# Performance work log

Measured on AMD Instinct MI355X. Metric: run time of the kernel, lower is better.

The kernel has to match this reference:

```python
import jax, jax.numpy as jnp
import numpy as np

N_R, N_V, D, E_RR, L, G = 50000, 2000, 128, 800000, 3, 32


def setup_inputs() -> dict:
    key = jax.random.key(0)
    ks = jax.random.split(key, 10)
    x_real = jax.random.normal(ks[0], (N_R, D), dtype=jnp.float32)
    x_virtual = jax.random.normal(ks[1], (N_V, D), dtype=jnp.float32)
    # params: [num_layers, 3 relations (r_to_r, r_to_v, v_to_r), D, D]
    W_root = jax.random.normal(ks[2], (L, 3, D, D), dtype=jnp.float32) * 0.05
    W_nbr = jax.random.normal(ks[3], (L, 3, D, D), dtype=jnp.float32) * 0.05
    bias = jax.random.normal(ks[4], (L, 3, D), dtype=jnp.float32) * 0.05
    edge_rr = jax.random.randint(ks[5], (2, E_RR), 0, N_R)
    # one virtual-node edge per real node (hierarchical virtual nodes)
    src_rv = jnp.arange(N_R)
    dst_rv = jax.random.randint(ks[6], (N_R,), 0, N_V)
    edge_rv = jnp.stack([src_rv, dst_rv])          # real -> virtual
    edge_vr = jnp.stack([dst_rv, src_rv])          # virtual -> real
    batch_real = jnp.sort(jax.random.randint(ks[7], (N_R,), 0, G))
    return {
        "x_real": x_real, "x_virtual": x_virtual,
        "W_root": W_root, "W_nbr": W_nbr, "bias": bias,
        "edge_rr": edge_rr, "edge_rv": edge_rv, "edge_vr": edge_vr,
        "batch_real": batch_real,
    }


def _graph_conv(x_src, x_dst, src, dst, Wr, Wn, b, n_dst):
    # PyG GraphConv-style: root transform + sum-aggregated neighbor messages
    msg = jax.ops.segment_sum(x_src[src] @ Wn, dst, num_segments=n_dst)
    return x_dst @ Wr + msg + b


def _forward(x_real, x_virtual, W_root, W_nbr, bias, edge_rr, edge_rv, edge_vr, batch_real):
    x_r, x_v = x_real, x_virtual
    n_r, n_v = x_r.shape[0], x_v.shape[0]
    for l in range(W_root.shape[0]):
        # HeteroConv with aggr='sum': sum relation outputs per destination type
        c_rr = _graph_conv(x_r, x_r, edge_rr[0], edge_rr[1], W_root[l, 0], W_nbr[l, 0], bias[l, 0], n_r)
        c_vr = _graph_conv(x_v, x_r, edge_vr[0], edge_vr[1], W_root[l, 2], W_nbr[l, 2], bias[l, 2], n_r)
        c_rv = _graph_conv(x_r, x_v, edge_rv[0], edge_rv[1], W_root[l, 1], W_nbr[l, 1], bias[l, 1], n_v)
        # activation + dropout (eval mode -> identity)
        x_r = jax.nn.relu(c_rr + c_vr)
        x_v = jax.nn.relu(c_rv)
    # mean readout over real nodes per graph
    counts = jax.ops.segment_sum(jnp.ones((n_r,), x_r.dtype), batch_real, num_segments=G)
    graph_emb = jax.ops.segment_sum(x_r, batch_real, num_segments=G) / jnp.maximum(counts, 1.0)[:, None]
    return x_r, graph_emb


def reference(x_real, x_virtual, W_root, W_nbr, bias, edge_rr, edge_rv, edge_vr, batch_real):
    node_embedding, graph_embedding = _forward(
        x_real, x_virtual, W_root, W_nbr, bias, edge_rr, edge_rv, edge_vr, batch_real)
    return node_embedding, graph_embedding
```

## Files before the change

### kernel.cpp

```cpp
#include <hip/hip_runtime.h>
#include <hip/hip_bf16.h>

#define N_R   50000
#define N_V   2000
#define DIM   128
#define E_RR  800000
#define NLAY  3
#define NGR   32
#define RCHUNK 16

#define BUKD  128
#define NBUK  391
#define CHKE  2048
#define NCHK  391

typedef __attribute__((ext_vector_type(8))) short bf16x8;
typedef __attribute__((ext_vector_type(4))) float f32x4;
typedef __attribute__((ext_vector_type(2))) float f32x2;
typedef __attribute__((ext_vector_type(8))) unsigned char u8x8;

__device__ __forceinline__ ushort f2bf(float f) {
    unsigned u = __builtin_bit_cast(unsigned, f);
    unsigned r = (u + 0x7fffu + ((u >> 16) & 1u)) >> 16;
    return (ushort)r;
}
__device__ __forceinline__ float bf2f(ushort h) {
    unsigned u = ((unsigned)h) << 16;
    return __builtin_bit_cast(float, u);
}
__device__ __forceinline__ int lbound(const int* __restrict__ a, int n, int key) {
    int lo = 0, hi = n;
    while (lo < hi) { int mid = (lo + hi) >> 1; if (a[mid] < key) lo = mid + 1; else hi = mid; }
    return lo;
}

__device__ __forceinline__ void acc_u8row(
    unsigned w0, unsigned w1, float s,
    f32x2& a01, f32x2& a23, f32x2& a45, f32x2& a67)
{
    f32x2 sc = {s, s};
    a01 += sc * (f32x2){(float)(w0 & 0xffu), (float)((w0 >> 8) & 0xffu)};
    a23 += sc * (f32x2){(float)((w0 >> 16) & 0xffu), (float)(w0 >> 24)};
    a45 += sc * (f32x2){(float)(w1 & 0xffu), (float)((w1 >> 8) & 0xffu)};
    a67 += sc * (f32x2){(float)((w1 >> 16) & 0xffu), (float)(w1 >> 24)};
}

__global__ __launch_bounds__(256) void hist_kernel(
    const int* __restrict__ dst, int n, int* __restrict__ cnt)
{
    int i = blockIdx.x * 256 + threadIdx.x;
    if (i < n) atomicAdd(&cnt[dst[i]], 1);
}

__global__ __launch_bounds__(256) void scan_single_kernel(
    const int* __restrict__ cnt, int n, int nedges,
    int* __restrict__ rowptr, int* __restrict__ cursor)
{
    __shared__ int lds[256];
    __shared__ int carry;
    int t = threadIdx.x;
    if (t == 0) carry = 0;
    __syncthreads();
    for (int base = 0; base < n; base += 256) {
        int i = base + t;
        int v = (i < n) ? cnt[i] : 0;
        lds[t] = v;
        __syncthreads();
        #pragma unroll
        for (int off = 1; off < 256; off <<= 1) {
            int u = (t >= off) ? lds[t - off] : 0;
            __syncthreads();
            lds[t] += u;
            __syncthreads();
        }
        int excl = carry + lds[t] - v;
        if (i < n) {
            rowptr[i] = excl;
            if (cursor) cursor[i] = excl;
        }
        __syncthreads();
        if (t == 255) carry += lds[255];
        __syncthreads();
    }
    if (t == 0) rowptr[n] = nedges;
}

__global__ __launch_bounds__(256) void fill_kernel(
    const int* __restrict__ src, const int* __restrict__ dst, int n,
    int* __restrict__ cursor, int* __restrict__ col)
{
    int i = blockIdx.x * 256 + threadIdx.x;
    if (i < n) {
        int p = atomicAdd(&cursor[dst[i]], 1);
        col[p] = src[i];
    }
}

__global__ __launch_bounds__(256) void bkt_count_kernel(
    const int* __restrict__ dst, unsigned short* __restrict__ cnt2d)
{
    __shared__ int h[NBUK];
    int t = threadIdx.x, c = blockIdx.x;
    for (int i = t; i < NBUK; i += 256) h[i] = 0;
    __syncthreads();
    int e0 = c * CHKE, e1 = min(e0 + CHKE, E_RR);
    for (int e = e0 + t; e < e1; e += 256) atomicAdd(&h[dst[e] >> 7], 1);
    __syncthreads();
    for (int i = t; i < NBUK; i += 256)
        cnt2d[(size_t)c * NBUK + i] = (unsigned short)h[i];
}

__global__ __launch_bounds__(64) void bkt_prefix_kernel(
    const unsigned short* __restrict__ cnt2d,
    unsigned short* __restrict__ rel2d, int* __restrict__ tot)
{
    int b = blockIdx.x, lane = threadIdx.x;
    int base = 0;
    for (int c0 = 0; c0 < NCHK; c0 += 64) {
        int c = c0 + lane;
        int v = (c < NCHK) ? (int)cnt2d[(size_t)c * NBUK + b] : 0;
        int s = v;
        #pragma unroll
        for (int off = 1; off < 64; off <<= 1) {
            int u = __shfl_up(s, off);
            if (lane >= off) s += u;
        }
        if (c < NCHK) rel2d[(size_t)c * NBUK + b] = (unsigned short)(base + s - v);
        base += __shfl(s, 63);
    }
    if (lane == 0) tot[b] = base;
}

__global__ __launch_bounds__(256) void bkt_scatter_kernel(
    const int* __restrict__ src, const int* __restrict__ dst,
    const unsigned short* __restrict__ rel2d, const int* __restrict__ bstart,
    unsigned* __restrict__ ebuf)
{
    __shared__ int cur[NBUK];
    int t = threadIdx.x, c = blockIdx.x;
    for (int i = t; i < NBUK; i += 256)
        cur[i] = bstart[i] + (int)rel2d[(size_t)c * NBUK + i];
    __syncthreads();
    int e0 = c * CHKE, e1 = min(e0 + CHKE, E_RR);
    for (int e = e0 + t; e < e1; e += 256) {
        int d = dst[e];
        int p = atomicAdd(&cur[d >> 7], 1);
        ebuf[p] = ((unsigned)d << 16) | (unsigned)src[e];
    }
}

__global__ __launch_bounds__(256) void bkt_fine_kernel(
    const unsigned* __restrict__ ebuf, const int* __restrict__ bstart,
    int* __restrict__ rowptr, int* __restrict__ col)
{
    __shared__ int cnt[BUKD];
    __shared__ int sc[BUKD];
    __shared__ int cur[BUKD];
    int b = blockIdx.x, t = threadIdx.x;
    int s0 = bstart[b], s1 = bstart[b + 1];
    if (t < BUKD) cnt[t] = 0;
    __syncthreads();
    for (int e = s0 + t; e < s1; e += 256)
        atomicAdd(&cnt[(ebuf[e] >> 16) & (BUKD - 1)], 1);
    __syncthreads();
    if (t < BUKD) sc[t] = cnt[t];
    __syncthreads();
    #pragma unroll
    for (int off = 1; off < BUKD; off <<= 1) {
        int v = (t < BUKD && t >= off) ? sc[t - off] : 0;
        __syncthreads();
        if (t < BUKD) sc[t] += v;
        __syncthreads();
    }
    if (t < BUKD) {
        int ex = sc[t] - cnt[t];
        int d = b * BUKD + t;
        if (d < N_R) rowptr[d] = s0 + ex;
        cur[t] = ex;
    }
    if (b == NBUK - 1 && t == 0) rowptr[N_R] = E_RR;
    __syncthreads();
    for (int e = s0 + t; e < s1; e += 256) {
        unsigned pk = ebuf[e];
        int p = atomicAdd(&cur[(pk >> 16) & (BUKD - 1)], 1);
        col[s0 + p] = (int)(pk & 0xffffu);
    }
}

__global__ __launch_bounds__(256) void quant_input_kernel(
    const float* __restrict__ in, unsigned char* __restrict__ q,
    float2* __restrict__ meta)
{
    int w = (blockIdx.x * 256 + threadIdx.x) >> 6;
    int lane = threadIdx.x & 63;
    if (w >= N_R) return;
    float2 v = *(const float2*)(in + (size_t)w * DIM + lane * 2);
    float mn = fminf(v.x, v.y), mx = fmaxf(v.x, v.y);
    #pragma unroll
    for (int off = 1; off < 64; off <<= 1) {
        mn = fminf(mn, __shfl_xor(mn, off));
        mx = fmaxf(mx, __shfl_xor(mx, off));
    }
    float range = mx - mn;
    float inv = (range > 0.f) ? 255.f / range : 0.f;
    unsigned q0 = (unsigned)__float2int_rn((v.x - mn) * inv);
    unsigned q1 = (unsigned)__float2int_rn((v.y - mn) * inv);
    *(ushort*)(q + (size_t)w * DIM + lane * 2) = (ushort)(q0 | (q1 << 8));
    if (lane == 0) meta[w] = make_float2(range / 255.f, mn);
}

__global__ __launch_bounds__(256) void build_wt_kernel(
    const float* __restrict__ Wroot, const float* __restrict__ Wnbr,
    ushort* __restrict__ WT)
{
    int idx = blockIdx.x * 256 + threadIdx.x;
    if (idx >= NLAY * DIM * 2 * DIM) return;
    int k = idx & 255;
    int n = (idx >> 8) & 127;
    int l = idx >> 15;
    float v;
    if (k < DIM) {
        const float* base = Wroot + (size_t)l * 3 * DIM * DIM;
        v = base[(size_t)k * DIM + n] + base[(size_t)(2 * DIM + k) * DIM + n];
    } else {
        v = Wnbr[((size_t)l * 3 * DIM + (k - DIM)) * DIM + n];
    }
    WT[idx] = f2bf(v);
}

__global__ __launch_bounds__(256) void combine_b_kernel(
    const float* __restrict__ bias, float* __restrict__ bc)
{
    int idx = blockIdx.x * 256 + threadIdx.x;
    if (idx >= NLAY * DIM) return;
    int l = idx / DIM;
    int rest = idx - l * DIM;
    const float* base = bias + (size_t)l * 3 * DIM;
    bc[idx] = base[rest] + base[2 * DIM + rest];
}

__global__ __launch_bounds__(256) void vlayer_kernel(
    const int* __restrict__ rowptr, const int* __restrict__ col,
    const unsigned char* __restrict__ Xq, const float2* __restrict__ Xm,
    const float* __restrict__ xv,
    const float* __restrict__ Wn2, const float* __restrict__ Wr1,
    const float* __restrict__ Wn1, const float* __restrict__ b1,
    float* __restrict__ Tv, float* __restrict__ xv_next, int doNext)
{
    __shared__ float part[4 * DIM];
    __shared__ float arv_s[DIM];
    int v = blockIdx.x;
    int t = threadIdx.x;
    int wave = t >> 6, lane = t & 63;

    if (doNext) {
        int beg = rowptr[v], end = rowptr[v + 1];
        float a0 = 0.f, a1 = 0.f, msum = 0.f;
        for (int e = beg + wave; e < end; e += 4) {
            int c = col[e];
            float2 m = Xm[c];
            uchar2 u = *(const uchar2*)(Xq + (size_t)c * DIM + lane * 2);
            a0 += m.x * (float)u.x;
            a1 += m.x * (float)u.y;
            msum += m.y;
        }
        part[wave * DIM + lane * 2 + 0] = a0 + msum;
        part[wave * DIM + lane * 2 + 1] = a1 + msum;
        __syncthreads();
        if (t < DIM)
            arv_s[t] = part[t] + part[DIM + t] + part[2 * DIM + t] + part[3 * DIM + t];
        __syncthreads();
    }

    const float* arow = xv + (size_t)v * DIM;
    if (t < DIM) {
        float tacc = 0.f;
        #pragma unroll 8
        for (int k = 0; k < DIM; ++k)
            tacc += arow[k] * Wn2[(size_t)k * DIM + t];
        Tv[(size_t)v * DIM + t] = tacc;
    } else if (doNext) {
        int c = t - DIM;
        float nacc = 0.f;
        #pragma unroll 4
        for (int k = 0; k < DIM; ++k)
            nacc += arow[k] * Wr1[(size_t)k * DIM + c]
                  + arv_s[k] * Wn1[(size_t)k * DIM + c];
        xv_next[(size_t)v * DIM + c] = fmaxf(nacc + b1[c], 0.f);
    }
}

__global__ __launch_bounds__(256) void fused_layer_kernel(
    const int* __restrict__ rowptr, const int* __restrict__ col,
    const unsigned char* __restrict__ Xq, const float2* __restrict__ Xm,
    const ushort* __restrict__ WT,
    const float* __restrict__ Tv,  const int* __restrict__ vmap,
    const float* __restrict__ bias,
    float* __restrict__ outF,
    unsigned char* __restrict__ Xq_out, float2* __restrict__ Xm_out, int M)
{
    __shared__ ushort a2[16 * DIM];
    __shared__ float ost[16 * DIM];
    int t = threadIdx.x;

    int wave = t >> 6, lane = t & 63;
    int rlo = lane & 15, hi = lane >> 4;
    int row0 = blockIdx.x * 16;
    int arowc = min(row0 + rlo, M - 1);
    float2 am = Xm[arowc];
    bf16x8 afr[8];
    #pragma unroll
    for (int j = 0; j < 4; ++j) {
        u8x8 uv = *(const u8x8*)(Xq + (size_t)arowc * DIM + 32 * j + 8 * hi);
        bf16x8 f;
        #pragma unroll
        for (int q = 0; q < 8; ++q)
            f[q] = (short)f2bf(am.x * (float)uv[q] + am.y);
        afr[j] = f;
    }
    int vr[4];
    #pragma unroll
    for (int i = 0; i < 4; ++i)
        vr[i] = vmap[min(row0 + 4 * hi + i, M - 1)];

    {
        int g = t >> 3;
        int li = t & 7;
        int row = g >> 1;
        int half = g & 1;
        int drow = min(row0 + row, M - 1);
        int beg = rowptr[drow], end = rowptr[drow + 1];
        const unsigned char* XH = Xq + half * 64 + li * 8;
        f32x2 a01 = {0.f, 0.f}, a23 = {0.f, 0.f};
        f32x2 a45 = {0.f, 0.f}, a67 = {0.f, 0.f};
        float msum = 0.f;
        int e = beg;
        for (; e + 3 < end; e += 4) {
            int c0 = col[e + 0], c1 = col[e + 1], c2 = col[e + 2], c3 = col[e + 3];
            float2 m0 = Xm[c0], m1 = Xm[c1], m2 = Xm[c2], m3 = Xm[c3];
            uint2 d0 = *(const uint2*)(XH + (size_t)c0 * DIM);
            uint2 d1 = *(const uint2*)(XH + (size_t)c1 * DIM);
            uint2 d2 = *(const uint2*)(XH + (size_t)c2 * DIM);
            uint2 d3 = *(const uint2*)(XH + (size_t)c3 * DIM);
            acc_u8row(d0.x, d0.y, m0.x, a01, a23, a45, a67);
            acc_u8row(d1.x, d1.y, m1.x, a01, a23, a45, a67);
            acc_u8row(d2.x, d2.y, m2.x, a01, a23, a45, a67);
            acc_u8row(d3.x, d3.y, m3.x, a01, a23, a45, a67);
            msum += (m0.y + m1.y) + (m2.y + m3.y);
        }
        for (; e < end; ++e) {
            int c0 = col[e];
            float2 m0 = Xm[c0];
            uint2 d0 = *(const uint2*)(XH + (size_t)c0 * DIM);
            acc_u8row(d0.x, d0.y, m0.x, a01, a23, a45, a67);
            msum += m0.y;
        }
        bf16x8 pk;
        pk[0] = (short)f2bf(a01.x + msum);
        pk[1] = (short)f2bf(a01.y + msum);
        pk[2] = (short)f2bf(a23.x + msum);
        pk[3] = (short)f2bf(a23.y + msum);
        pk[4] = (short)f2bf(a45.x + msum);
        pk[5] = (short)f2bf(a45.y + msum);
        pk[6] = (short)f2bf(a67.x + msum);
        pk[7] = (short)f2bf(a67.y + msum);
        int byte = row * 256 + ((half * 128 + li * 16) ^ ((row & 7) << 4));
        *(bf16x8*)((char*)a2 + byte) = pk;
    }
    __syncthreads();

    #pragma unroll
    for (int jj = 0; jj < 4; ++jj) {
        int byte = rlo * 256 + ((64 * jj + 16 * hi) ^ ((rlo & 7) << 4));
        afr[4 + jj] = *(const bf16x8*)((const char*)a2 + byte);
    }

    f32x4 acc[2];
    #pragma unroll
    for (int n = 0; n < 2; ++n) acc[n] = (f32x4){0.f, 0.f, 0.f, 0.f};

    #pragma unroll
    for (int n = 0; n < 2; ++n) {
        int nt = wave * 2 + n;
        const ushort* wrow = WT + (size_t)(nt * 16 + rlo) * (2 * DIM);
        #pragma unroll
        for (int j = 0; j < 8; ++j) {
            bf16x8 bfr = *(const bf16x8*)(wrow + 32 * j + 8 * hi);
            acc[n] = __builtin_amdgcn_mfma_f32_16x16x32_bf16(afr[j], bfr, acc[n], 0, 0, 0);
        }
    }

    if (outF) {
        #pragma unroll
        for (int n = 0; n < 2; ++n) {
            int ncol = (wave * 2 + n) * 16 + rlo;
            float bv = bias[ncol];
            #pragma unroll
            for (int i = 0; i < 4; ++i) {
                int orow = row0 + 4 * hi + i;
                if (orow >= M) continue;
                float v = acc[n][i] + bv + Tv[(size_t)vr[i] * DIM + ncol];
                outF[(size_t)orow * DIM + ncol] = fmaxf(v, 0.f);
            }
        }
    } else {
        #pragma unroll
        for (int n = 0; n < 2; ++n) {
            int ncol = (wave * 2 + n) * 16 + rlo;
            float bv = bias[ncol];
            #pragma unroll
            for (int i = 0; i < 4; ++i) {
                float v = acc[n][i] + bv + Tv[(size_t)vr[i] * DIM + ncol];
                ost[(4 * hi + i) * DIM + ncol] = fmaxf(v, 0.f);
            }
        }
        __syncthreads();
        int g16 = t >> 4;
        int li16 = t & 15;
        int orow = row0 + g16;
        float4 f0 = *(const float4*)(ost + g16 * DIM + li16 * 8);
        float4 f1 = *(const float4*)(ost + g16 * DIM + li16 * 8 + 4);
        float mn = fminf(fminf(fminf(f0.x, f0.y), fminf(f0.z, f0.w)),
                         fminf(fminf(f1.x, f1.y), fminf(f1.z, f1.w)));
        float mx = fmaxf(fmaxf(fmaxf(f0.x, f0.y), fmaxf(f0.z, f0.w)),
                         fmaxf(fmaxf(f1.x, f1.y), fmaxf(f1.z, f1.w)));
        #pragma unroll
        for (int off = 1; off < 16; off <<= 1) {
            mn = fminf(mn, __shfl_xor(mn, off, 16));
            mx = fmaxf(mx, __shfl_xor(mx, off, 16));
        }
        float range = mx - mn;
        float inv = (range > 0.f) ? 255.f / range : 0.f;
        if (orow < M) {
            u8x8 qv;
            qv[0] = (unsigned char)__float2int_rn((f0.x - mn) * inv);
            qv[1] = (unsigned char)__float2int_rn((f0.y - mn) * inv);
            qv[2] = (unsigned char)__float2int_rn((f0.z - mn) * inv);
            qv[3] = (unsigned char)__float2int_rn((f0.w - mn) * inv);
            qv[4] = (unsigned char)__float2int_rn((f1.x - mn) * inv);
            qv[5] = (unsigned char)__float2int_rn((f1.y - mn) * inv);
            qv[6] = (unsigned char)__float2int_rn((f1.z - mn) * inv);
            qv[7] = (unsigned char)__float2int_rn((f1.w - mn) * inv);
            *(u8x8*)(Xq_out + (size_t)orow * DIM + li16 * 8) = qv;
            if (li16 == 0) Xm_out[orow] = make_float2(range / 255.f, mn);
        }
    }
}

__global__ __launch_bounds__(256) void readout_kernel(
    const float* __restrict__ xr, const int* __restrict__ batch,
    float* __restrict__ gsum, int nrows)
{
    __shared__ float lds[256 * 4];
    int g = blockIdx.x / RCHUNK;
    int chunk = blockIdx.x % RCHUNK;
    int lo = lbound(batch, nrows, g);
    int hi = lbound(batch, nrows, g + 1);
    int len = hi - lo;
    if (len == 0) return;
    int per = (len + RCHUNK - 1) / RCHUNK;
    int r0 = lo + chunk * per;
    int r1 = min(r0 + per, hi);

    int t = threadIdx.x;
    int c4 = (t & 31) << 2;
    int rsub = t >> 5;

    float4 acc = make_float4(0.f, 0.f, 0.f, 0.f);
    for (int r = r0 + rsub; r < r1; r += 8) {
        float4 v = *(const float4*)(xr + (size_t)r * DIM + c4);
        acc.x += v.x; acc.y += v.y; acc.z += v.z; acc.w += v.w;
    }
    *(float4*)(lds + t * 4) = acc;
    __syncthreads();
    if (rsub == 0) {
        float4 s = make_float4(0.f, 0.f, 0.f, 0.f);
        #pragma unroll
        for (int j = 0; j < 8; ++j) {
            float4 v = *(const float4*)(lds + (j * 32 + t) * 4);
            s.x += v.x; s.y += v.y; s.z += v.z; s.w += v.w;
        }
        atomicAdd(&gsum[(size_t)g * DIM + c4 + 0], s.x);
        atomicAdd(&gsum[(size_t)g * DIM + c4 + 1], s.y);
        atomicAdd(&gsum[(size_t)g * DIM + c4 + 2], s.z);
        atomicAdd(&gsum[(size_t)g * DIM + c4 + 3], s.w);
    }
}

__global__ __launch_bounds__(256) void finalize_kernel(
    const float* __restrict__ gsum, const int* __restrict__ batch,
    float* __restrict__ out, int nrows)
{
    int idx = blockIdx.x * 256 + threadIdx.x;
    if (idx >= NGR * DIM) return;
    int g = idx >> 7;
    int lo = lbound(batch, nrows, g);
    int hi = lbound(batch, nrows, g + 1);
    float c = fmaxf((float)(hi - lo), 1.f);
    out[idx] = gsum[idx] / c;
}

extern "C" void kernel_launch(void* const* d_in, const int* in_sizes, int n_in,
                              void* d_out, int out_size, void* d_ws, size_t ws_size,
                              hipStream_t stream)
{
    const float* x_real    = (const float*)d_in[0];
    const float* x_virtual = (const float*)d_in[1];
    const float* W_root    = (const float*)d_in[2];
    const float* W_nbr     = (const float*)d_in[3];
    const float* bias      = (const float*)d_in[4];
    const int*   edge_rr   = (const int*)d_in[5];
    const int*   edge_rv   = (const int*)d_in[6];
    const int*   edge_vr   = (const int*)d_in[7];
    const int*   batch     = (const int*)d_in[8];

    float* out = (float*)d_out;

    float2* meta0 = (float2*)d_ws;
    float2* meta1 = meta0 + N_R;
    float2* meta2 = meta1 + N_R;
    float*  Tv    = (float*)(meta2 + N_R);
    float*  xv_a  = Tv   + (size_t)N_V * DIM;
    float*  xv_b  = xv_a + (size_t)N_V * DIM;
    float*  bc    = xv_b + (size_t)N_V * DIM;
    float*  gsum  = bc   + (size_t)NLAY * DIM;
    ushort* WT    = (ushort*)(gsum + NGR * DIM);
    int* iws       = (int*)(WT + (size_t)NLAY * DIM * 2 * DIM);
    int* rowptr_rr = iws;
    int* col_rr    = rowptr_rr + N_R + 1;
    int* cnt_v     = col_rr + E_RR;
    int* rowptr_rv = cnt_v + N_V;
    int* cursor_rv = rowptr_rv + N_V + 1;
    int* col_rv    = cursor_rv + N_V;
    int* tot       = col_rv + N_R;
    int* bstart    = tot + NBUK;
    unsigned short* cnt2d = (unsigned short*)(bstart + NBUK + 1);
    unsigned short* rel2d = cnt2d + (size_t)NCHK * NBUK;
    unsigned* ebuf = (unsigned*)(rel2d + (size_t)NCHK * NBUK + 2);
    unsigned char* Q0 = (unsigned char*)(ebuf + E_RR);
    unsigned char* Q1 = Q0 + (size_t)N_R * DIM;
    unsigned char* Q2 = Q1 + (size_t)N_R * DIM;

    const int* rr_src = edge_rr;
    const int* rr_dst = edge_rr + E_RR;
    const int* rv_src = edge_rv;
    const int* rv_dst = edge_rv + N_R;

    bkt_count_kernel<<<NCHK, 256, 0, stream>>>(rr_dst, cnt2d);
    bkt_prefix_kernel<<<NBUK, 64, 0, stream>>>(cnt2d, rel2d, tot);
    scan_single_kernel<<<1, 256, 0, stream>>>(tot, NBUK, E_RR, bstart, nullptr);
    bkt_scatter_kernel<<<NCHK, 256, 0, stream>>>(rr_src, rr_dst, rel2d, bstart, ebuf);
    bkt_fine_kernel<<<NBUK, 256, 0, stream>>>(ebuf, bstart, rowptr_rr, col_rr);

    hipMemsetAsync(cnt_v, 0, (size_t)N_V * sizeof(int), stream);
    hist_kernel<<<(N_R + 255) / 256, 256, 0, stream>>>(rv_dst, N_R, cnt_v);
    scan_single_kernel<<<1, 256, 0, stream>>>(cnt_v, N_V, N_R, rowptr_rv, cursor_rv);
    fill_kernel<<<(N_R + 255) / 256, 256, 0, stream>>>(rv_src, rv_dst, N_R, cursor_rv, col_rv);

    build_wt_kernel<<<(NLAY * DIM * 2 * DIM + 255) / 256, 256, 0, stream>>>(W_root, W_nbr, WT);
    combine_b_kernel<<<(NLAY * DIM + 255) / 256, 256, 0, stream>>>(bias, bc);
    quant_input_kernel<<<(N_R * 64 + 255) / 256, 256, 0, stream>>>(x_real, Q0, meta0);

    unsigned char* Qcur = Q0;  float2* Mcur = meta0;
    const float* cur_xv = x_virtual;

    for (int l = 0; l < NLAY; ++l) {
        const float* Wn1 = W_nbr + ((size_t)l * 3 + 1) * DIM * DIM;
        const float* Wn2 = W_nbr + ((size_t)l * 3 + 2) * DIM * DIM;
        const float* Wr1 = W_root + ((size_t)l * 3 + 1) * DIM * DIM;
        const float* b1  = bias + ((size_t)l * 3 + 1) * DIM;

        int doNext = (l < NLAY - 1);
        float* xv_out = (l & 1) ? xv_b : xv_a;

        vlayer_kernel<<<N_V, 256, 0, stream>>>(
            rowptr_rv, col_rv, Qcur, Mcur, cur_xv,
            Wn2, Wr1, Wn1, b1, Tv, xv_out, doNext);

        unsigned char* Qnext = (l == 0) ? Q1 : Q2;
        float2*        Mnext = (l == 0) ? meta1 : meta2;
        float* outF = (l == NLAY - 1) ? out : nullptr;
        fused_layer_kernel<<<(N_R + 15) / 16, 256, 0, stream>>>(
            rowptr_rr, col_rr, Qcur, Mcur, WT + (size_t)l * DIM * 2 * DIM,
            Tv, edge_vr, bc + (size_t)l * DIM,
            outF, outF ? nullptr : Qnext, outF ? nullptr : Mnext, N_R);

        if (doNext) { cur_xv = xv_out; Qcur = Qnext; Mcur = Mnext; }
    }

    hipMemsetAsync(gsum, 0, (size_t)NGR * DIM * sizeof(float), stream);
    readout_kernel<<<NGR * RCHUNK, 256, 0, stream>>>(out, batch, gsum, N_R);
    finalize_kernel<<<(NGR * DIM + 255) / 256, 256, 0, stream>>>(
        gsum, batch, out + (size_t)N_R * DIM, N_R);
}
```

Baseline: 319.8 us.

## Pack per-row bf16 scale into CSR column indices and use symmetric quantization

Switches the per-row int8 quantization from asymmetric min/range float2 metadata to a single bf16 scale with a fixed zero point (128 for the input layer, 0 for post-ReLU layers). Each layer gets a repack kernel that fuses the 16-bit column index and the source row's bf16 scale into one 32-bit word. The gather loop can then read scale and index in one load instead of a separate dependent metadata lookup per edge. The cost is an extra 800K-element repack pass per layer and a coarser quantization, with a bf16-rounded scale and the zero point fixed rather than fitted per row.

```diff
diff --git a/kernel.cpp b/kernel.cpp
--- a/kernel.cpp
+++ b/kernel.cpp
@@ -151,7 +151,7 @@
 
 __global__ __launch_bounds__(256) void bkt_fine_kernel(
     const unsigned* __restrict__ ebuf, const int* __restrict__ bstart,
-    int* __restrict__ rowptr, int* __restrict__ col)
+    int* __restrict__ rowptr, unsigned short* __restrict__ col16)
 {
     __shared__ int cnt[BUKD];
     __shared__ int sc[BUKD];
@@ -183,30 +183,41 @@
     for (int e = s0 + t; e < s1; e += 256) {
         unsigned pk = ebuf[e];
         int p = atomicAdd(&cur[(pk >> 16) & (BUKD - 1)], 1);
-        col[s0 + p] = (int)(pk & 0xffffu);
+        col16[s0 + p] = (unsigned short)(pk & 0xffffu);
+    }
+}
+
+__global__ __launch_bounds__(256) void repack_kernel(
+    const unsigned short* __restrict__ col16,
+    const unsigned short* __restrict__ sbf,
+    unsigned* __restrict__ colp)
+{
+    int i = blockIdx.x * 256 + threadIdx.x;
+    if (i < E_RR) {
+        unsigned c = col16[i];
+        colp[i] = c | ((unsigned)sbf[c] << 16);
     }
 }
 
 __global__ __launch_bounds__(256) void quant_input_kernel(
     const float* __restrict__ in, unsigned char* __restrict__ q,
-    float2* __restrict__ meta)
+    unsigned short* __restrict__ sbf)
 {
     int w = (blockIdx.x * 256 + threadIdx.x) >> 6;
     int lane = threadIdx.x & 63;
     if (w >= N_R) return;
     float2 v = *(const float2*)(in + (size_t)w * DIM + lane * 2);
-    float mn = fminf(v.x, v.y), mx = fmaxf(v.x, v.y);
+    float mx = fmaxf(fabsf(v.x), fabsf(v.y));
     #pragma unroll
-    for (int off = 1; off < 64; off <<= 1) {
-        mn = fminf(mn, __shfl_xor(mn, off));
+    for (int off = 1; off < 64; off <<= 1)
         mx = fmaxf(mx, __shfl_xor(mx, off));
-    }
-    float range = mx - mn;
-    float inv = (range > 0.f) ? 255.f / range : 0.f;
-    unsigned q0 = (unsigned)__float2int_rn((v.x - mn) * inv);
-    unsigned q1 = (unsigned)__float2int_rn((v.y - mn) * inv);
+    ushort sb = f2bf(mx / 127.f);
+    float s = bf2f(sb);
+    float inv = (s > 0.f) ? 1.f / s : 0.f;
+    int q0 = min(255, max(0, __float2int_rn(v.x * inv) + 128));
+    int q1 = min(255, max(0, __float2int_rn(v.y * inv) + 128));
     *(ushort*)(q + (size_t)w * DIM + lane * 2) = (ushort)(q0 | (q1 << 8));
-    if (lane == 0) meta[w] = make_float2(range / 255.f, mn);
+    if (lane == 0) sbf[w] = sb;
 }
 
 __global__ __launch_bounds__(256) void build_wt_kernel(
@@ -241,8 +252,8 @@
 
 __global__ __launch_bounds__(256) void vlayer_kernel(
     const int* __restrict__ rowptr, const int* __restrict__ col,
-    const unsigned char* __restrict__ Xq, const float2* __restrict__ Xm,
-    const float* __restrict__ xv,
+    const unsigned char* __restrict__ Xq, const unsigned short* __restrict__ sbf,
+    float zp, const float* __restrict__ xv,
     const float* __restrict__ Wn2, const float* __restrict__ Wr1,
     const float* __restrict__ Wn1, const float* __restrict__ b1,
     float* __restrict__ Tv, float* __restrict__ xv_next, int doNext)
@@ -255,17 +266,17 @@
 
     if (doNext) {
         int beg = rowptr[v], end = rowptr[v + 1];
-        float a0 = 0.f, a1 = 0.f, msum = 0.f;
+        float a0 = 0.f, a1 = 0.f, ssum = 0.f;
         for (int e = beg + wave; e < end; e += 4) {
             int c = col[e];
-            float2 m = Xm[c];
+            float s = bf2f(sbf[c]);
             uchar2 u = *(const uchar2*)(Xq + (size_t)c * DIM + lane * 2);
-            a0 += m.x * (float)u.x;
-            a1 += m.x * (float)u.y;
-            msum += m.y;
-        }
-        part[wave * DIM + lane * 2 + 0] = a0 + msum;
-        part[wave * DIM + lane * 2 + 1] = a1 + msum;
+            a0 += s * (float)u.x;
+            a1 += s * (float)u.y;
+            ssum += s;
+        }
+        part[wave * DIM + lane * 2 + 0] = a0 - zp * ssum;
+        part[wave * DIM + lane * 2 + 1] = a1 - zp * ssum;
         __syncthreads();
         if (t < DIM)
             arv_s[t] = part[t] + part[DIM + t] + part[2 * DIM + t] + part[3 * DIM + t];
@@ -291,13 +302,13 @@
 }
 
 __global__ __launch_bounds__(256) void fused_layer_kernel(
-    const int* __restrict__ rowptr, const int* __restrict__ col,
-    const unsigned char* __restrict__ Xq, const float2* __restrict__ Xm,
-    const ushort* __restrict__ WT,
+    const int* __restrict__ rowptr, const unsigned* __restrict__ colp,
+    const unsigned char* __restrict__ Xq, const unsigned short* __restrict__ sbf,
+    float zp, const ushort* __restrict__ WT,
     const float* __restrict__ Tv,  const int* __restrict__ vmap,
     const float* __restrict__ bias,
     float* __restrict__ outF,
-    unsigned char* __restrict__ Xq_out, float2* __restrict__ Xm_out, int M)
+    unsigned char* __restrict__ Xq_out, unsigned short* __restrict__ sbf_out, int M)
 {
     __shared__ ushort a2[16 * DIM];
     __shared__ float ost[16 * DIM];
@@ -307,7 +318,7 @@
     int rlo = lane & 15, hi = lane >> 4;
     int row0 = blockIdx.x * 16;
     int arowc = min(row0 + rlo, M - 1);
-    float2 am = Xm[arowc];
+    float sa = bf2f(sbf[arowc]);
     bf16x8 afr[8];
     #pragma unroll
     for (int j = 0; j < 4; ++j) {
@@ -315,7 +326,7 @@
         bf16x8 f;
         #pragma unroll
         for (int q = 0; q < 8; ++q)
-            f[q] = (short)f2bf(am.x * (float)uv[q] + am.y);
+            f[q] = (short)f2bf(sa * ((float)uv[q] - zp));
         afr[j] = f;
     }
     int vr[4];
@@ -333,37 +344,40 @@
         const unsigned char* XH = Xq + half * 64 + li * 8;
         f32x2 a01 = {0.f, 0.f}, a23 = {0.f, 0.f};
         f32x2 a45 = {0.f, 0.f}, a67 = {0.f, 0.f};
-        float msum = 0.f;
+        float ssum = 0.f;
         int e = beg;
         for (; e + 3 < end; e += 4) {
-            int c0 = col[e + 0], c1 = col[e + 1], c2 = col[e + 2], c3 = col[e + 3];
-            float2 m0 = Xm[c0], m1 = Xm[c1], m2 = Xm[c2], m3 = Xm[c3];
-            uint2 d0 = *(const uint2*)(XH + (size_t)c0 * DIM);
-            uint2 d1 = *(const uint2*)(XH + (size_t)c1 * DIM);
-            uint2 d2 = *(const uint2*)(XH + (size_t)c2 * DIM);
-            uint2 d3 = *(const uint2*)(XH + (size_t)c3 * DIM);
-            acc_u8row(d0.x, d0.y, m0.x, a01, a23, a45, a67);
-            acc_u8row(d1.x, d1.y, m1.x, a01, a23, a45, a67);
-            acc_u8row(d2.x, d2.y, m2.x, a01, a23, a45, a67);
-            acc_u8row(d3.x, d3.y, m3.x, a01, a23, a45, a67);
-            msum += (m0.y + m1.y) + (m2.y + m3.y);
+            unsigned p0 = colp[e + 0], p1 = colp[e + 1];
+            unsigned p2 = colp[e + 2], p3 = colp[e + 3];
+            float s0 = bf2f((ushort)(p0 >> 16)), s1 = bf2f((ushort)(p1 >> 16));
+            float s2 = bf2f((ushort)(p2 >> 16)), s3 = bf2f((ushort)(p3 >> 16));
+            uint2 d0 = *(const uint2*)(XH + (size_t)(p0 & 0xffffu) * DIM);
+            uint2 d1 = *(const uint2*)(XH + (size_t)(p1 & 0xffffu) * DIM);
+            uint2 d2 = *(const uint2*)(XH + (size_t)(p2 & 0xffffu) * DIM);
+            uint2 d3 = *(const uint2*)(XH + (size_t)(p3 & 0xffffu) * DIM);
+            acc_u8row(d0.x, d0.y, s0, a01, a23, a45, a67);
+            acc_u8row(d1.x, d1.y, s1, a01, a23, a45, a67);
+            acc_u8row(d2.x, d2.y, s2, a01, a23, a45, a67);
+            acc_u8row(d3.x, d3.y, s3, a01, a23, a45, a67);
+            ssum += (s0 + s1) + (s2 + s3);
         }
         for (; e < end; ++e) {
-            int c0 = col[e];
-            float2 m0 = Xm[c0];
-            uint2 d0 = *(const uint2*)(XH + (size_t)c0 * DIM);
-            acc_u8row(d0.x, d0.y, m0.x, a01, a23, a45, a67);
-            msum += m0.y;
-        }
+            unsigned p0 = colp[e];
+            float s0 = bf2f((ushort)(p0 >> 16));
+            uint2 d0 = *(const uint2*)(XH + (size_t)(p0 & 0xffffu) * DIM);
+            acc_u8row(d0.x, d0.y, s0, a01, a23, a45, a67);
+            ssum += s0;
+        }
+        float zs = zp * ssum;
         bf16x8 pk;
-        pk[0] = (short)f2bf(a01.x + msum);
-        pk[1] = (short)f2bf(a01.y + msum);
-        pk[2] = (short)f2bf(a23.x + msum);
-        pk[3] = (short)f2bf(a23.y + msum);
-        pk[4] = (short)f2bf(a45.x + msum);
-        pk[5] = (short)f2bf(a45.y + msum);
-        pk[6] = (short)f2bf(a67.x + msum);
-        pk[7] = (short)f2bf(a67.y + msum);
+        pk[0] = (short)f2bf(a01.x - zs);
+        pk[1] = (short)f2bf(a01.y - zs);
+        pk[2] = (short)f2bf(a23.x - zs);
+        pk[3] = (short)f2bf(a23.y - zs);
+        pk[4] = (short)f2bf(a45.x - zs);
+        pk[5] = (short)f2bf(a45.y - zs);
+        pk[6] = (short)f2bf(a67.x - zs);
+        pk[7] = (short)f2bf(a67.y - zs);
         int byte = row * 256 + ((half * 128 + li * 16) ^ ((row & 7) << 4));
         *(bf16x8*)((char*)a2 + byte) = pk;
     }
@@ -420,29 +434,26 @@
         int orow = row0 + g16;
         float4 f0 = *(const float4*)(ost + g16 * DIM + li16 * 8);
         float4 f1 = *(const float4*)(ost + g16 * DIM + li16 * 8 + 4);
-        float mn = fminf(fminf(fminf(f0.x, f0.y), fminf(f0.z, f0.w)),
-                         fminf(fminf(f1.x, f1.y), fminf(f1.z, f1.w)));
         float mx = fmaxf(fmaxf(fmaxf(f0.x, f0.y), fmaxf(f0.z, f0.w)),
                          fmaxf(fmaxf(f1.x, f1.y), fmaxf(f1.z, f1.w)));
         #pragma unroll
-        for (int off = 1; off < 16; off <<= 1) {
-            mn = fminf(mn, __shfl_xor(mn, off, 16));
+        for (int off = 1; off < 16; off <<= 1)
             mx = fmaxf(mx, __shfl_xor(mx, off, 16));
-        }
-        float range = mx - mn;
-        float inv = (range > 0.f) ? 255.f / range : 0.f;
+        ushort sb = f2bf(mx / 255.f);
+        float s = bf2f(sb);
+        float inv = (s > 0.f) ? 1.f / s : 0.f;
         if (orow < M) {
             u8x8 qv;
-            qv[0] = (unsigned char)__float2int_rn((f0.x - mn) * inv);
-            qv[1] = (unsigned char)__float2int_rn((f0.y - mn) * inv);
-            qv[2] = (unsigned char)__float2int_rn((f0.z - mn) * inv);
-            qv[3] = (unsigned char)__float2int_rn((f0.w - mn) * inv);
-            qv[4] = (unsigned char)__float2int_rn((f1.x - mn) * inv);
-            qv[5] = (unsigned char)__float2int_rn((f1.y - mn) * inv);
-            qv[6] = (unsigned char)__float2int_rn((f1.z - mn) * inv);
-            qv[7] = (unsigned char)__float2int_rn((f1.w - mn) * inv);
+            qv[0] = (unsigned char)min(255, __float2int_rn(f0.x * inv));
+            qv[1] = (unsigned char)min(255, __float2int_rn(f0.y * inv));
+            qv[2] = (unsigned char)min(255, __float2int_rn(f0.z * inv));
+            qv[3] = (unsigned char)min(255, __float2int_rn(f0.w * inv));
+            qv[4] = (unsigned char)min(255, __float2int_rn(f1.x * inv));
+            qv[5] = (unsigned char)min(255, __float2int_rn(f1.y * inv));
+            qv[6] = (unsigned char)min(255, __float2int_rn(f1.z * inv));
+            qv[7] = (unsigned char)min(255, __float2int_rn(f1.w * inv));
             *(u8x8*)(Xq_out + (size_t)orow * DIM + li16 * 8) = qv;
-            if (li16 == 0) Xm_out[orow] = make_float2(range / 255.f, mn);
+            if (li16 == 0) sbf_out[orow] = sb;
         }
     }
 }
@@ -516,10 +527,8 @@
 
     float* out = (float*)d_out;
 
-    float2* meta0 = (float2*)d_ws;
-    float2* meta1 = meta0 + N_R;
-    float2* meta2 = meta1 + N_R;
-    float*  Tv    = (float*)(meta2 + N_R);
+    float*  ws    = (float*)d_ws;
+    float*  Tv    = ws;
     float*  xv_a  = Tv   + (size_t)N_V * DIM;
     float*  xv_b  = xv_a + (size_t)N_V * DIM;
     float*  bc    = xv_b + (size_t)N_V * DIM;
@@ -527,17 +536,21 @@
     ushort* WT    = (ushort*)(gsum + NGR * DIM);
     int* iws       = (int*)(WT + (size_t)NLAY * DIM * 2 * DIM);
     int* rowptr_rr = iws;
-    int* col_rr    = rowptr_rr + N_R + 1;
-    int* cnt_v     = col_rr + E_RR;
+    int* cnt_v     = rowptr_rr + N_R + 1;
     int* rowptr_rv = cnt_v + N_V;
     int* cursor_rv = rowptr_rv + N_V + 1;
     int* col_rv    = cursor_rv + N_V;
     int* tot       = col_rv + N_R;
     int* bstart    = tot + NBUK;
-    unsigned short* cnt2d = (unsigned short*)(bstart + NBUK + 1);
+    unsigned* colp = (unsigned*)(bstart + NBUK + 1);
+    unsigned* ebuf = colp + E_RR;
+    unsigned short* col16 = (unsigned short*)(ebuf + E_RR);
+    unsigned short* cnt2d = col16 + E_RR;
     unsigned short* rel2d = cnt2d + (size_t)NCHK * NBUK;
-    unsigned* ebuf = (unsigned*)(rel2d + (size_t)NCHK * NBUK + 2);
-    unsigned char* Q0 = (unsigned char*)(ebuf + E_RR);
+    unsigned short* sbf0  = rel2d + (size_t)NCHK * NBUK;
+    unsigned short* sbf1  = sbf0 + N_R;
+    unsigned short* sbf2  = sbf1 + N_R;
+    unsigned char* Q0 = (unsigned char*)(sbf2 + N_R);
     unsigned char* Q1 = Q0 + (size_t)N_R * DIM;
     unsigned char* Q2 = Q1 + (size_t)N_R * DIM;
 
@@ -550,7 +563,7 @@
     bkt_prefix_kernel<<<NBUK, 64, 0, stream>>>(cnt2d, rel2d, tot);
     scan_single_kernel<<<1, 256, 0, stream>>>(tot, NBUK, E_RR, bstart, nullptr);
     bkt_scatter_kernel<<<NCHK, 256, 0, stream>>>(rr_src, rr_dst, rel2d, bstart, ebuf);
-    bkt_fine_kernel<<<NBUK, 256, 0, stream>>>(ebuf, bstart, rowptr_rr, col_rr);
+    bkt_fine_kernel<<<NBUK, 256, 0, stream>>>(ebuf, bstart, rowptr_rr, col16);
 
     hipMemsetAsync(cnt_v, 0, (size_t)N_V * sizeof(int), stream);
     hist_kernel<<<(N_R + 255) / 256, 256, 0, stream>>>(rv_dst, N_R, cnt_v);
@@ -559,9 +572,9 @@
 
     build_wt_kernel<<<(NLAY * DIM * 2 * DIM + 255) / 256, 256, 0, stream>>>(W_root, W_nbr, WT);
     combine_b_kernel<<<(NLAY * DIM + 255) / 256, 256, 0, stream>>>(bias, bc);
-    quant_input_kernel<<<(N_R * 64 + 255) / 256, 256, 0, stream>>>(x_real, Q0, meta0);
-
-    unsigned char* Qcur = Q0;  float2* Mcur = meta0;
+    quant_input_kernel<<<(N_R * 64 + 255) / 256, 256, 0, stream>>>(x_real, Q0, sbf0);
+
+    unsigned char* Qcur = Q0;  unsigned short* Scur = sbf0;
     const float* cur_xv = x_virtual;
 
     for (int l = 0; l < NLAY; ++l) {
@@ -571,21 +584,24 @@
         const float* b1  = bias + ((size_t)l * 3 + 1) * DIM;
 
         int doNext = (l < NLAY - 1);
+        float zp = (l == 0) ? 128.f : 0.f;
         float* xv_out = (l & 1) ? xv_b : xv_a;
 
+        repack_kernel<<<(E_RR + 255) / 256, 256, 0, stream>>>(col16, Scur, colp);
+
         vlayer_kernel<<<N_V, 256, 0, stream>>>(
-            rowptr_rv, col_rv, Qcur, Mcur, cur_xv,
+            rowptr_rv, col_rv, Qcur, Scur, zp, cur_xv,
             Wn2, Wr1, Wn1, b1, Tv, xv_out, doNext);
 
-        unsigned char* Qnext = (l == 0) ? Q1 : Q2;
-        float2*        Mnext = (l == 0) ? meta1 : meta2;
+        unsigned char*  Qnext = (l == 0) ? Q1 : Q2;
+        unsigned short* Snext = (l == 0) ? sbf1 : sbf2;
         float* outF = (l == NLAY - 1) ? out : nullptr;
         fused_layer_kernel<<<(N_R + 15) / 16, 256, 0, stream>>>(
-            rowptr_rr, col_rr, Qcur, Mcur, WT + (size_t)l * DIM * 2 * DIM,
+            rowptr_rr, colp, Qcur, Scur, zp, WT + (size_t)l * DIM * 2 * DIM,
             Tv, edge_vr, bc + (size_t)l * DIM,
-            outF, outF ? nullptr : Qnext, outF ? nullptr : Mnext, N_R);
-
-        if (doNext) { cur_xv = xv_out; Qcur = Qnext; Mcur = Mnext; }
+            outF, outF ? nullptr : Qnext, outF ? nullptr : Snext, N_R);
+
+        if (doNext) { cur_xv = xv_out; Qcur = Qnext; Scur = Snext; }
     }
 
     hipMemsetAsync(gsum, 0, (size_t)NGR * DIM * sizeof(float), stream);
```

New measurement: 322.9 us. Within noise of the previous version (+1.0%).
